# Kernel tuning notes

Hardware: AMD Instinct MI355X
Metric: run time of the kernel (lower is better)

The kernel has to match this reference:

```python
import jax, jax.numpy as jnp
import numpy as np

N_NODES = 50000
N_EDGES = 800000
F_IN = 32
H = 128
LN_EPS = 1e-5


def _gcn_layer(h, src, tgt, w_self, b_self, w_neigh, b_neigh):
    # h: [N, D]; src/tgt: [E]
    n = h.shape[0]
    self_feat = h @ w_self + b_self                      # [N, Dout]
    src_feat = h[src]                                    # [E, D] gather
    agg = jax.ops.segment_sum(src_feat, tgt, num_segments=n)          # [N, D]
    cnt = jax.ops.segment_sum(jnp.ones((src.shape[0],), h.dtype), tgt,
                              num_segments=n)[:, None]   # [N, 1]
    agg = agg / jnp.maximum(cnt, 1.0)
    return self_feat + agg @ w_neigh + b_neigh


def _layer_norm(x, gamma, beta):
    mu = jnp.mean(x, axis=-1, keepdims=True)
    var = jnp.mean(jnp.square(x - mu), axis=-1, keepdims=True)
    return (x - mu) * jax.lax.rsqrt(var + LN_EPS) * gamma + beta


def setup_inputs() -> dict:
    key = jax.random.key(0)
    ks = jax.random.split(key, 16)
    s_in = 1.0 / np.sqrt(F_IN)
    s_h = 1.0 / np.sqrt(H)
    inp = {
        "x": jax.random.normal(ks[0], (N_NODES, F_IN), jnp.float32),
        "edge_index": jax.random.randint(ks[1], (2, N_EDGES), 0, N_NODES, jnp.int64)
        if jax.config.jax_enable_x64 else
        jax.random.randint(ks[1], (2, N_EDGES), 0, N_NODES, jnp.int32),
        "w_in": jax.random.uniform(ks[2], (F_IN, H), jnp.float32, -s_in, s_in),
        "b_in": jax.random.uniform(ks[3], (H,), jnp.float32, -s_in, s_in),
        "ws0": jax.random.uniform(ks[4], (H, H), jnp.float32, -s_h, s_h),
        "bs0": jax.random.uniform(ks[5], (H,), jnp.float32, -s_h, s_h),
        "wn0": jax.random.uniform(ks[6], (H, H), jnp.float32, -s_h, s_h),
        "bn0": jax.random.uniform(ks[7], (H,), jnp.float32, -s_h, s_h),
        "g0": jnp.ones((H,), jnp.float32),
        "be0": jnp.zeros((H,), jnp.float32),
        "ws1": jax.random.uniform(ks[8], (H, H), jnp.float32, -s_h, s_h),
        "bs1": jax.random.uniform(ks[9], (H,), jnp.float32, -s_h, s_h),
        "wn1": jax.random.uniform(ks[10], (H, H), jnp.float32, -s_h, s_h),
        "bn1": jax.random.uniform(ks[11], (H,), jnp.float32, -s_h, s_h),
        "g1": jnp.ones((H,), jnp.float32),
        "be1": jnp.zeros((H,), jnp.float32),
    }
    return inp


def reference(x, edge_index, w_in, b_in, ws0, bs0, wn0, bn0, g0, be0,
              ws1, bs1, wn1, bn1, g1, be1):
    src, tgt = edge_index[0], edge_index[1]
    h = jax.nn.relu(x @ w_in + b_in)                     # input_proj + relu
    # layer 0 (intermediate): gcn -> LN -> relu -> dropout(eval=id) -> residual
    residual = h
    h = _gcn_layer(h, src, tgt, ws0, bs0, wn0, bn0)
    h = _layer_norm(h, g0, be0)
    h = jax.nn.relu(h) + residual
    # layer 1 (final): gcn -> LN
    h = _gcn_layer(h, src, tgt, ws1, bs1, wn1, bn1)
    h = _layer_norm(h, g1, be1)
    return h
```

## Files before the change

kernel.cpp:

```cpp
#include <hip/hip_runtime.h>

#define H 128
#define CAP 64
#define FLS 16
typedef unsigned short ushort_t;
typedef __bf16 bf16x8 __attribute__((ext_vector_type(8)));
typedef unsigned short u16x8 __attribute__((ext_vector_type(8)));
typedef float f32x4 __attribute__((ext_vector_type(4)));
typedef float f32x2 __attribute__((ext_vector_type(2)));
typedef int i32x4 __attribute__((ext_vector_type(4)));

__device__ __forceinline__ float bf2f(ushort_t b) {
    return __uint_as_float(((unsigned int)b) << 16);
}
__device__ __forceinline__ ushort_t f2bf(float f) {
    unsigned int u = __float_as_uint(f);
    unsigned int r = (u + 0x7fffu + ((u >> 16) & 1u)) >> 16;
    return (ushort_t)r;
}
__device__ __forceinline__ unsigned char f2fp8(float f) {
    int r = __builtin_amdgcn_cvt_pk_fp8_f32(f, f, 0, false);
    return (unsigned char)(r & 0xff);
}
__device__ __forceinline__ void acc8(float* s, uint2 v) {
    f32x2 a0 = __builtin_amdgcn_cvt_pk_f32_fp8(v.x, false);
    f32x2 a1 = __builtin_amdgcn_cvt_pk_f32_fp8(v.x, true);
    f32x2 a2 = __builtin_amdgcn_cvt_pk_f32_fp8(v.y, false);
    f32x2 a3 = __builtin_amdgcn_cvt_pk_f32_fp8(v.y, true);
    s[0] += a0.x; s[1] += a0.y; s[2] += a1.x; s[3] += a1.y;
    s[4] += a2.x; s[5] += a2.y; s[6] += a3.x; s[7] += a3.y;
}

__device__ __forceinline__
void pack_one(int idx, const float* __restrict__ W0, const float* __restrict__ W1,
              const float* __restrict__ b0, const float* __restrict__ b1,
              ushort_t* __restrict__ Wpack, float* __restrict__ bsum,
              int Ksplit, int K)
{
    int total = K * 16;
    if (idx < total) {
        int l = idx & 63, tt = (idx >> 6) & 7, s = idx >> 9;
        int c = tt * 16 + (l & 15);
        int kb = s * 32 + ((l >> 4) & 3) * 8;
#pragma unroll
        for (int j = 0; j < 8; ++j) {
            int k = kb + j;
            float v = (k < Ksplit) ? W0[(size_t)k * H + c]
                                   : W1[(size_t)(k - Ksplit) * H + c];
            Wpack[(size_t)idx * 8 + j] = f2bf(v);
        }
    }
    if (idx < H) bsum[idx] = b0[idx] + (b1 ? b1[idx] : 0.f);
}

__global__ __launch_bounds__(256)
void k_prep(const float* __restrict__ w_in, const float* __restrict__ b_in,
            const float* __restrict__ ws0, const float* __restrict__ bs0,
            const float* __restrict__ wn0, const float* __restrict__ bn0,
            const float* __restrict__ ws1, const float* __restrict__ bs1,
            const float* __restrict__ wn1, const float* __restrict__ bn1,
            ushort_t* __restrict__ Wpin, float* __restrict__ bin,
            ushort_t* __restrict__ Wp0, float* __restrict__ bsm0,
            ushort_t* __restrict__ Wp1, float* __restrict__ bsm1,
            int* __restrict__ fl, int N)
{
    int b = blockIdx.x, t = threadIdx.x;
    if (b < 2) {
        pack_one(b * 256 + t, w_in, w_in, b_in, nullptr, Wpin, bin, 32, 32);
    } else if (b < 18) {
        pack_one((b - 2) * 256 + t, ws0, wn0, bs0, bn0, Wp0, bsm0, 128, 256);
    } else if (b < 34) {
        pack_one((b - 18) * 256 + t, ws1, wn1, bs1, bn1, Wp1, bsm1, 128, 256);
    } else {
        int i = (b - 34) * 256 + t;
        if (i < N) fl[i * FLS] = 0;
    }
}

#define FILL_CHUNK 4096

__device__ __forceinline__
void fill_body(int blk, const int* __restrict__ srcs, const int* __restrict__ tgts,
               int* __restrict__ fl, ushort_t* __restrict__ col, int E)
{
    int range = blk & 7;
    int chunk = blk >> 3;
    int base = chunk * FILL_CHUNK;
    int t = threadIdx.x;
    int i0 = base + t * 4;
    i32x4 tg[4], sr[4];
#pragma unroll
    for (int u = 0; u < 4; ++u) {
        int idx = i0 + u * 1024;
        if (idx + 3 < E) {
            tg[u] = __builtin_nontemporal_load((const i32x4*)(tgts + idx));
            sr[u] = __builtin_nontemporal_load((const i32x4*)(srcs + idx));
        } else {
            i32x4 v = {-1, -1, -1, -1}, s = {0, 0, 0, 0};
#pragma unroll
            for (int j = 0; j < 4; ++j)
                if (idx + j < E) { v[j] = tgts[idx + j]; s[j] = srcs[idx + j]; }
            tg[u] = v; sr[u] = s;
        }
    }
#pragma unroll
    for (int u = 0; u < 4; ++u) {
#pragma unroll
        for (int j = 0; j < 4; ++j) {
            int tt = tg[u][j];
            if (tt >= 0 && (tt >> 13) == range) {
                int p = atomicAdd(&fl[tt * FLS], 1);
                if (p < CAP) col[tt * CAP + p] = (ushort_t)sr[u][j];
            }
        }
    }
}

template<int K, int DO_LN, int RESREL, int RELU, int OUTBF, int HQ, int AF32>
__device__ __forceinline__
void gemm_body(int bidm,
               const ushort_t* __restrict__ A, const float* __restrict__ Af, int lda,
               const ushort_t* __restrict__ Wpack,
               const float* __restrict__ bias,
               const float* __restrict__ g, const float* __restrict__ be,
               const ushort_t* __restrict__ resid, int ldr,
               float* __restrict__ Cf, ushort_t* __restrict__ Cb,
               unsigned char* __restrict__ hq, int ldc, int M)
{
    constexpr int NS = K / 32;
    __shared__ ushort_t Bs[NS * 8 * 64 * 8];
    const int t = threadIdx.x;
    {
        const uint4* wsrc = (const uint4*)Wpack;
        uint4* wdst = (uint4*)Bs;
        constexpr int CH = K * 16;
#pragma unroll
        for (int i = t; i < CH; i += 256) wdst[i] = wsrc[i];
    }
    __syncthreads();

    const int wave = t >> 6, lane = t & 63;
    const int quad = lane >> 4, l16 = lane & 15;
    const int m0 = bidm * 128 + wave * 32;

    f32x4 acc[2][8];
#pragma unroll
    for (int mt = 0; mt < 2; ++mt)
#pragma unroll
        for (int nt = 0; nt < 8; ++nt) acc[mt][nt] = (f32x4){0.f, 0.f, 0.f, 0.f};

    bf16x8 afrag[NS][2];
#pragma unroll
    for (int s = 0; s < NS; ++s)
#pragma unroll
        for (int mt = 0; mt < 2; ++mt) {
            int row = m0 + mt * 16 + l16;
            if (row >= M) row = M - 1;
            if (AF32) {
                const float* p = Af + (size_t)row * lda + s * 32 + quad * 8;
                float4 v0 = *(const float4*)p;
                float4 v1 = *(const float4*)(p + 4);
                union { u16x8 u; bf16x8 b; } cv;
                cv.u[0] = f2bf(v0.x); cv.u[1] = f2bf(v0.y);
                cv.u[2] = f2bf(v0.z); cv.u[3] = f2bf(v0.w);
                cv.u[4] = f2bf(v1.x); cv.u[5] = f2bf(v1.y);
                cv.u[6] = f2bf(v1.z); cv.u[7] = f2bf(v1.w);
                afrag[s][mt] = cv.b;
            } else {
                afrag[s][mt] = *(const bf16x8*)(A + (size_t)row * lda + s * 32 + quad * 8);
            }
        }

    const bf16x8* bfr = (const bf16x8*)Bs;
#pragma unroll
    for (int s = 0; s < NS; ++s)
#pragma unroll
        for (int nt = 0; nt < 8; ++nt) {
            bf16x8 b = bfr[(s * 8 + nt) * 64 + lane];
#pragma unroll
            for (int mt = 0; mt < 2; ++mt)
                acc[mt][nt] = __builtin_amdgcn_mfma_f32_16x16x32_bf16(
                    afrag[s][mt], b, acc[mt][nt], 0, 0, 0);
        }

    float bv[8], gv[8], bev[8];
#pragma unroll
    for (int nt = 0; nt < 8; ++nt) {
        int c = nt * 16 + l16;
        bv[nt] = bias[c];
        if (DO_LN) { gv[nt] = g[c]; bev[nt] = be[c]; }
    }

#pragma unroll
    for (int mt = 0; mt < 2; ++mt)
#pragma unroll
        for (int r = 0; r < 4; ++r) {
            int row = m0 + mt * 16 + quad * 4 + r;
            float v[8];
#pragma unroll
            for (int nt = 0; nt < 8; ++nt) v[nt] = acc[mt][nt][r] + bv[nt];
            if (DO_LN) {
                float s1 = 0.f, s2 = 0.f;
#pragma unroll
                for (int nt = 0; nt < 8; ++nt) { s1 += v[nt]; s2 += v[nt] * v[nt]; }
#pragma unroll
                for (int mk = 1; mk < 16; mk <<= 1) {
                    s1 += __shfl_xor(s1, mk);
                    s2 += __shfl_xor(s2, mk);
                }
                float mu = s1 * (1.f / H);
                float var = s2 * (1.f / H) - mu * mu;
                float rs = rsqrtf(var + 1e-5f);
#pragma unroll
                for (int nt = 0; nt < 8; ++nt)
                    v[nt] = (v[nt] - mu) * rs * gv[nt] + bev[nt];
            }
            if (row < M) {
#pragma unroll
                for (int nt = 0; nt < 8; ++nt) {
                    int c = nt * 16 + l16;
                    float y = v[nt];
                    if (RELU) y = fmaxf(y, 0.f);
                    if (RESREL)
                        y = fmaxf(y, 0.f) + bf2f(resid[(size_t)row * ldr + c]);
                    if (OUTBF) Cb[(size_t)row * ldc + c] = f2bf(y);
                    else       Cf[(size_t)row * ldc + c] = y;
                    if (HQ) hq[(size_t)row * H + c] = f2fp8(y);
                }
            }
        }
}

__global__ __launch_bounds__(256)
void k_gin(const float* __restrict__ x, const ushort_t* __restrict__ Wpin,
           const float* __restrict__ bin,
           ushort_t* __restrict__ Cb, unsigned char* __restrict__ hq,
           const int* __restrict__ srcs, const int* __restrict__ tgts,
           int* __restrict__ fl, ushort_t* __restrict__ col, int E,
           int fillBlocks, int M)
{
    if ((int)blockIdx.x < fillBlocks) {
        fill_body(blockIdx.x, srcs, tgts, fl, col, E);
        return;
    }
    gemm_body<32, 0, 0, 1, 1, 1, 1>(blockIdx.x - fillBlocks,
        nullptr, x, 32, Wpin, bin, nullptr, nullptr, nullptr, 0,
        nullptr, Cb, hq, 256, M);
}

__global__ __launch_bounds__(256)
void k_gl0(const ushort_t* __restrict__ A, const ushort_t* __restrict__ Wp,
           const float* __restrict__ bias,
           const float* __restrict__ g, const float* __restrict__ be,
           ushort_t* __restrict__ Cb, unsigned char* __restrict__ hq, int M)
{
    gemm_body<256, 1, 1, 0, 1, 1, 0>(blockIdx.x,
        A, nullptr, 256, Wp, bias, g, be, A, 256,
        nullptr, Cb, hq, 256, M);
}

__global__ __launch_bounds__(256)
void k_gl1(const ushort_t* __restrict__ A, const ushort_t* __restrict__ Wp,
           const float* __restrict__ bias,
           const float* __restrict__ g, const float* __restrict__ be,
           float* __restrict__ Cf, int M)
{
    gemm_body<256, 1, 0, 0, 0, 0, 0>(blockIdx.x,
        A, nullptr, 256, Wp, bias, g, be, nullptr, 0,
        Cf, nullptr, nullptr, H, M);
}

__device__ __forceinline__
void agg_body(const unsigned char* __restrict__ hq, const int* __restrict__ fl,
              const ushort_t* __restrict__ col, ushort_t* __restrict__ out, int n)
{
    int node = blockIdx.x * 4 + (threadIdx.x >> 6);
    if (node >= n) return;
    int lane = threadIdx.x & 63;
    int grp = lane >> 4, li = lane & 15;
    int cnt = fl[node * FLS];
    int m = cnt < CAP ? cnt : CAP;
    int beg = node * CAP, end = beg + m;
    float s[8];
#pragma unroll
    for (int j = 0; j < 8; ++j) s[j] = 0.f;

    int e = beg;
    for (; e + 16 <= end; e += 16) {
        uint2 v[4];
#pragma unroll
        for (int q = 0; q < 4; ++q) {
            int r = col[e + 4 * q + grp];
            v[q] = *(const uint2*)(hq + (size_t)r * 128 + li * 8);
        }
#pragma unroll
        for (int q = 0; q < 4; ++q) acc8(s, v[q]);
    }
    if (e + 8 <= end) {
        uint2 v[2];
#pragma unroll
        for (int q = 0; q < 2; ++q) {
            int r = col[e + 4 * q + grp];
            v[q] = *(const uint2*)(hq + (size_t)r * 128 + li * 8);
        }
#pragma unroll
        for (int q = 0; q < 2; ++q) acc8(s, v[q]);
        e += 8;
    }
    if (e + 4 <= end) {
        int r = col[e + grp];
        uint2 v0 = *(const uint2*)(hq + (size_t)r * 128 + li * 8);
        acc8(s, v0);
        e += 4;
    }
    for (; e < end; ++e) {
        if (grp == 0) {
            int r = col[e];
            uint2 v0 = *(const uint2*)(hq + (size_t)r * 128 + li * 8);
            acc8(s, v0);
        }
    }
#pragma unroll
    for (int j = 0; j < 8; ++j) {
        s[j] += __shfl_xor(s[j], 16);
        s[j] += __shfl_xor(s[j], 32);
    }
    if (grp == 0) {
        float inv = 1.f / fmaxf((float)cnt, 1.f);
        uint4 o;
        o.x = ((unsigned)f2bf(s[1] * inv) << 16) | f2bf(s[0] * inv);
        o.y = ((unsigned)f2bf(s[3] * inv) << 16) | f2bf(s[2] * inv);
        o.z = ((unsigned)f2bf(s[5] * inv) << 16) | f2bf(s[4] * inv);
        o.w = ((unsigned)f2bf(s[7] * inv) << 16) | f2bf(s[6] * inv);
        *(uint4*)(out + (size_t)node * 256 + li * 8) = o;
    }
}

__global__ __launch_bounds__(256)
void k_agg0(const unsigned char* __restrict__ hq, const int* __restrict__ fl,
            const ushort_t* __restrict__ col, ushort_t* __restrict__ out, int n)
{ agg_body(hq, fl, col, out, n); }

__global__ __launch_bounds__(256)
void k_agg1(const unsigned char* __restrict__ hq, const int* __restrict__ fl,
            const ushort_t* __restrict__ col, ushort_t* __restrict__ out, int n)
{ agg_body(hq, fl, col, out, n); }

extern "C" void kernel_launch(void* const* d_in, const int* in_sizes, int n_in,
                              void* d_out, int out_size, void* d_ws, size_t ws_size,
                              hipStream_t stream)
{
    const float* x    = (const float*)d_in[0];
    const int*   ei   = (const int*)d_in[1];
    const float* w_in = (const float*)d_in[2];
    const float* b_in = (const float*)d_in[3];
    const float* ws0  = (const float*)d_in[4];
    const float* bs0  = (const float*)d_in[5];
    const float* wn0  = (const float*)d_in[6];
    const float* bn0  = (const float*)d_in[7];
    const float* g0   = (const float*)d_in[8];
    const float* be0  = (const float*)d_in[9];
    const float* ws1  = (const float*)d_in[10];
    const float* bs1  = (const float*)d_in[11];
    const float* wn1  = (const float*)d_in[12];
    const float* bn1  = (const float*)d_in[13];
    const float* g1   = (const float*)d_in[14];
    const float* be1  = (const float*)d_in[15];

    const int N = in_sizes[0] / 32;
    const int E = in_sizes[1] / 2;
    const int* srcs = ei;
    const int* tgts = ei + E;

    char* w = (char*)d_ws;
    ushort_t* Acat0 = (ushort_t*)w;  w += (size_t)N * 256 * 2;
    ushort_t* Acat1 = (ushort_t*)w;  w += (size_t)N * 256 * 2;
    unsigned char* hq0 = (unsigned char*)w;  w += (size_t)N * H;
    unsigned char* hq1 = (unsigned char*)w;  w += (size_t)N * H;
    ushort_t* Wpin  = (ushort_t*)w;  w += 32 * H * 2;
    ushort_t* Wp0   = (ushort_t*)w;  w += 256 * H * 2;
    ushort_t* Wp1   = (ushort_t*)w;  w += 256 * H * 2;
    float* bin  = (float*)w;         w += H * 4;
    float* bsm0 = (float*)w;         w += H * 4;
    float* bsm1 = (float*)w;         w += H * 4;
    int* fl     = (int*)w;           w += (size_t)N * FLS * 4;
    ushort_t* col = (ushort_t*)w;    w += (size_t)N * CAP * 2;

    int gN = (N + 255) / 256;
    int gM = (N + 127) / 128;
    int gF = 8 * ((E + FILL_CHUNK - 1) / FILL_CHUNK);

    k_prep<<<34 + gN, 256, 0, stream>>>(
        w_in, b_in, ws0, bs0, wn0, bn0, ws1, bs1, wn1, bn1,
        Wpin, bin, Wp0, bsm0, Wp1, bsm1, fl, N);

    k_gin<<<gF + gM, 256, 0, stream>>>(
        x, Wpin, bin, Acat0, hq0, srcs, tgts, fl, col, E, gF, N);

    k_agg0<<<(N + 3) / 4, 256, 0, stream>>>(hq0, fl, col, Acat0 + 128, N);
    k_gl0<<<gM, 256, 0, stream>>>(Acat0, Wp0, bsm0, g0, be0, Acat1, hq1, N);

    k_agg1<<<(N + 3) / 4, 256, 0, stream>>>(hq1, fl, col, Acat1 + 128, N);
    k_gl1<<<gM, 256, 0, stream>>>(Acat1, Wp1, bsm1, g1, be1, (float*)d_out, N);
}
```

Baseline: 231.0 us.

## Read GEMM weights from global, halve row tile, and batch fill atomics

The layer GEMMs no longer stage the 64KB packed weight matrix in LDS. They read B fragments straight from global memory through the cache, each wave handles 16 rows instead of 32, and the grid doubles. This removes the per-block LDS fill, the barrier, and the occupancy limit set by 64KB of LDS, at the cost of more global/L2 traffic for weights. The CSR fill uses half-size chunks and issues all its atomics before any column writes, so more atomics are in flight per thread.

```diff
diff --git a/kernel.cpp b/kernel.cpp
--- a/kernel.cpp
+++ b/kernel.cpp
@@ -77,7 +77,7 @@
     }
 }
 
-#define FILL_CHUNK 4096
+#define FILL_CHUNK 2048
 
 __device__ __forceinline__
 void fill_body(int blk, const int* __restrict__ srcs, const int* __restrict__ tgts,
@@ -88,35 +88,38 @@
     int base = chunk * FILL_CHUNK;
     int t = threadIdx.x;
     int i0 = base + t * 4;
-    i32x4 tg[4], sr[4];
-#pragma unroll
-    for (int u = 0; u < 4; ++u) {
+    int tgv[8], srv[8];
+#pragma unroll
+    for (int u = 0; u < 2; ++u) {
         int idx = i0 + u * 1024;
+        i32x4 tg, sr;
         if (idx + 3 < E) {
-            tg[u] = __builtin_nontemporal_load((const i32x4*)(tgts + idx));
-            sr[u] = __builtin_nontemporal_load((const i32x4*)(srcs + idx));
+            tg = __builtin_nontemporal_load((const i32x4*)(tgts + idx));
+            sr = __builtin_nontemporal_load((const i32x4*)(srcs + idx));
         } else {
             i32x4 v = {-1, -1, -1, -1}, s = {0, 0, 0, 0};
 #pragma unroll
             for (int j = 0; j < 4; ++j)
                 if (idx + j < E) { v[j] = tgts[idx + j]; s[j] = srcs[idx + j]; }
-            tg[u] = v; sr[u] = s;
-        }
-    }
-#pragma unroll
-    for (int u = 0; u < 4; ++u) {
-#pragma unroll
-        for (int j = 0; j < 4; ++j) {
-            int tt = tg[u][j];
-            if (tt >= 0 && (tt >> 13) == range) {
-                int p = atomicAdd(&fl[tt * FLS], 1);
-                if (p < CAP) col[tt * CAP + p] = (ushort_t)sr[u][j];
-            }
-        }
-    }
-}
-
-template<int K, int DO_LN, int RESREL, int RELU, int OUTBF, int HQ, int AF32>
+            tg = v; sr = s;
+        }
+#pragma unroll
+        for (int j = 0; j < 4; ++j) { tgv[u * 4 + j] = tg[j]; srv[u * 4 + j] = sr[j]; }
+    }
+    int p[8];
+#pragma unroll
+    for (int k = 0; k < 8; ++k) {
+        int tt = tgv[k];
+        bool m = (tt >= 0) && ((tt >> 13) == range);
+        p[k] = m ? atomicAdd(&fl[tt * FLS], 1) : CAP;
+    }
+#pragma unroll
+    for (int k = 0; k < 8; ++k)
+        if (p[k] < CAP) col[tgv[k] * CAP + p[k]] = (ushort_t)srv[k];
+}
+
+template<int K, int MT, int STAGEB, int DO_LN, int RESREL, int RELU,
+         int OUTBF, int HQ, int AF32>
 __device__ __forceinline__
 void gemm_body(int bidm,
                const ushort_t* __restrict__ A, const float* __restrict__ Af, int lda,
@@ -128,32 +131,36 @@
                unsigned char* __restrict__ hq, int ldc, int M)
 {
     constexpr int NS = K / 32;
-    __shared__ ushort_t Bs[NS * 8 * 64 * 8];
     const int t = threadIdx.x;
-    {
+    const bf16x8* bfr;
+    if constexpr (STAGEB) {
+        __shared__ ushort_t Bs[NS * 8 * 64 * 8];
         const uint4* wsrc = (const uint4*)Wpack;
         uint4* wdst = (uint4*)Bs;
         constexpr int CH = K * 16;
 #pragma unroll
         for (int i = t; i < CH; i += 256) wdst[i] = wsrc[i];
-    }
-    __syncthreads();
+        __syncthreads();
+        bfr = (const bf16x8*)Bs;
+    } else {
+        bfr = (const bf16x8*)Wpack;
+    }
 
     const int wave = t >> 6, lane = t & 63;
     const int quad = lane >> 4, l16 = lane & 15;
-    const int m0 = bidm * 128 + wave * 32;
-
-    f32x4 acc[2][8];
-#pragma unroll
-    for (int mt = 0; mt < 2; ++mt)
+    const int m0 = bidm * (MT * 64) + wave * (MT * 16);
+
+    f32x4 acc[MT][8];
+#pragma unroll
+    for (int mt = 0; mt < MT; ++mt)
 #pragma unroll
         for (int nt = 0; nt < 8; ++nt) acc[mt][nt] = (f32x4){0.f, 0.f, 0.f, 0.f};
 
-    bf16x8 afrag[NS][2];
+    bf16x8 afrag[NS][MT];
 #pragma unroll
     for (int s = 0; s < NS; ++s)
 #pragma unroll
-        for (int mt = 0; mt < 2; ++mt) {
+        for (int mt = 0; mt < MT; ++mt) {
             int row = m0 + mt * 16 + l16;
             if (row >= M) row = M - 1;
             if (AF32) {
@@ -171,17 +178,29 @@
             }
         }
 
-    const bf16x8* bfr = (const bf16x8*)Bs;
-#pragma unroll
-    for (int s = 0; s < NS; ++s)
-#pragma unroll
-        for (int nt = 0; nt < 8; ++nt) {
-            bf16x8 b = bfr[(s * 8 + nt) * 64 + lane];
-#pragma unroll
-            for (int mt = 0; mt < 2; ++mt)
-                acc[mt][nt] = __builtin_amdgcn_mfma_f32_16x16x32_bf16(
-                    afrag[s][mt], b, acc[mt][nt], 0, 0, 0);
-        }
+    if constexpr (STAGEB) {
+#pragma unroll
+        for (int s = 0; s < NS; ++s)
+#pragma unroll
+            for (int nt = 0; nt < 8; ++nt) {
+                bf16x8 b = bfr[(s * 8 + nt) * 64 + lane];
+#pragma unroll
+                for (int mt = 0; mt < MT; ++mt)
+                    acc[mt][nt] = __builtin_amdgcn_mfma_f32_16x16x32_bf16(
+                        afrag[s][mt], b, acc[mt][nt], 0, 0, 0);
+            }
+    } else {
+#pragma unroll 1
+        for (int s = 0; s < NS; ++s)
+#pragma unroll
+            for (int nt = 0; nt < 8; ++nt) {
+                bf16x8 b = bfr[(s * 8 + nt) * 64 + lane];
+#pragma unroll
+                for (int mt = 0; mt < MT; ++mt)
+                    acc[mt][nt] = __builtin_amdgcn_mfma_f32_16x16x32_bf16(
+                        afrag[s][mt], b, acc[mt][nt], 0, 0, 0);
+            }
+    }
 
     float bv[8], gv[8], bev[8];
 #pragma unroll
@@ -192,7 +211,7 @@
     }
 
 #pragma unroll
-    for (int mt = 0; mt < 2; ++mt)
+    for (int mt = 0; mt < MT; ++mt)
 #pragma unroll
         for (int r = 0; r < 4; ++r) {
             int row = m0 + mt * 16 + quad * 4 + r;
@@ -243,7 +262,7 @@
         fill_body(blockIdx.x, srcs, tgts, fl, col, E);
         return;
     }
-    gemm_body<32, 0, 0, 1, 1, 1, 1>(blockIdx.x - fillBlocks,
+    gemm_body<32, 2, 1, 0, 0, 1, 1, 1, 1>(blockIdx.x - fillBlocks,
         nullptr, x, 32, Wpin, bin, nullptr, nullptr, nullptr, 0,
         nullptr, Cb, hq, 256, M);
 }
@@ -254,7 +273,7 @@
            const float* __restrict__ g, const float* __restrict__ be,
            ushort_t* __restrict__ Cb, unsigned char* __restrict__ hq, int M)
 {
-    gemm_body<256, 1, 1, 0, 1, 1, 0>(blockIdx.x,
+    gemm_body<256, 1, 0, 1, 1, 0, 1, 1, 0>(blockIdx.x,
         A, nullptr, 256, Wp, bias, g, be, A, 256,
         nullptr, Cb, hq, 256, M);
 }
@@ -265,7 +284,7 @@
            const float* __restrict__ g, const float* __restrict__ be,
            float* __restrict__ Cf, int M)
 {
-    gemm_body<256, 1, 0, 0, 0, 0, 0>(blockIdx.x,
+    gemm_body<256, 1, 0, 1, 0, 0, 0, 0, 0>(blockIdx.x,
         A, nullptr, 256, Wp, bias, g, be, nullptr, 0,
         Cf, nullptr, nullptr, H, M);
 }
@@ -387,19 +406,20 @@
     ushort_t* col = (ushort_t*)w;    w += (size_t)N * CAP * 2;
 
     int gN = (N + 255) / 256;
-    int gM = (N + 127) / 128;
+    int gMi = (N + 127) / 128;
+    int gMg = (N + 63) / 64;
     int gF = 8 * ((E + FILL_CHUNK - 1) / FILL_CHUNK);
 
     k_prep<<<34 + gN, 256, 0, stream>>>(
         w_in, b_in, ws0, bs0, wn0, bn0, ws1, bs1, wn1, bn1,
         Wpin, bin, Wp0, bsm0, Wp1, bsm1, fl, N);
 
-    k_gin<<<gF + gM, 256, 0, stream>>>(
+    k_gin<<<gF + gMi, 256, 0, stream>>>(
         x, Wpin, bin, Acat0, hq0, srcs, tgts, fl, col, E, gF, N);
 
     k_agg0<<<(N + 3) / 4, 256, 0, stream>>>(hq0, fl, col, Acat0 + 128, N);
-    k_gl0<<<gM, 256, 0, stream>>>(Acat0, Wp0, bsm0, g0, be0, Acat1, hq1, N);
+    k_gl0<<<gMg, 256, 0, stream>>>(Acat0, Wp0, bsm0, g0, be0, Acat1, hq1, N);
 
     k_agg1<<<(N + 3) / 4, 256, 0, stream>>>(hq1, fl, col, Acat1 + 128, N);
-    k_gl1<<<gM, 256, 0, stream>>>(Acat1, Wp1, bsm1, g1, be1, (float*)d_out, N);
-}
+    k_gl1<<<gMg, 256, 0, stream>>>(Acat1, Wp1, bsm1, g1, be1, (float*)d_out, N);
+}
```

Measured after the change: 437.6 us. 1.89x slower.
